# Kernel tuning notes

Hardware: AMD Instinct MI355X
Metric: run time of the kernel (lower is better)

Reference implementation:

```python
import jax, jax.numpy as jnp
import numpy as np

H, W, C = 768, 768, 64


def _segment_ids(mask):
    """mask: [L] int binary separator mask -> [L] int32 segment ids.
    A new grid segment starts at each rising edge (0 -> 1) of the mask;
    pixel 0 always belongs to segment 0. Equivalent to GridStructureBuilder's
    run-based row/column partition, derived via a single cumsum."""
    m = mask.astype(jnp.int32)
    prev = jnp.concatenate([jnp.zeros((1,), jnp.int32), m[:-1]])
    rising = ((m == 1) & (prev == 0)).at[0].set(False)
    return jnp.cumsum(rising.astype(jnp.int32))


def setup_inputs() -> dict:
    key = jax.random.key(0)
    k1, k2, k3 = jax.random.split(key, 3)
    return {
        "input": jax.random.normal(k1, (1, H, W, C), dtype=jnp.float32),
        "h_mask": jax.random.randint(k2, (1, H), 0, 2, dtype=jnp.int32),
        "v_mask": jax.random.randint(k3, (1, W), 0, 2, dtype=jnp.int32),
    }


def reference(input, h_mask, v_mask):
    x = input[0]                      # [H, W, C]
    h, w, c = x.shape
    row_ids = _segment_ids(h_mask[0])  # [H]
    col_ids = _segment_ids(v_mask[0])  # [W]
    # flat cell id per pixel; w is a static upper bound on the column count
    idx = (row_ids[:, None] * w + col_ids[None, :]).reshape(-1)  # [H*W]
    xf = x.reshape(h * w, c)
    n_seg = h * w                      # static upper bound on cell count
    sums = jax.ops.segment_sum(xf, idx, num_segments=n_seg)           # [n_seg, C]
    counts = jax.ops.segment_sum(jnp.ones((h * w,), x.dtype), idx,
                                 num_segments=n_seg)                  # [n_seg]
    # scatter-add of (1/area)*x == per-cell mean
    means = sums / jnp.maximum(counts, 1.0)[:, None]
    # keep_size=True: gather cell means back to every pixel
    return means[idx].reshape(1, h, w, c)
```

## Files before the change

kernel.cpp:

```cpp
#include <hip/hip_runtime.h>


#define GH 768
#define GW 768
#define GC 64
#define MAXSEG 385

enum {
    OFF_ROWSTART = 0,
    OFF_ROWEND   = OFF_ROWSTART + MAXSEG,
    OFF_COLSTART = OFF_ROWEND + MAXSEG,
    OFF_COLEND   = OFF_COLSTART + MAXSEG,
    OFF_NROWS    = OFF_COLEND + MAXSEG,
    OFF_NCOLS    = OFF_NROWS + 1,
};

__global__ __launch_bounds__(768) void seg_scan(const int* __restrict__ h_mask,
                                                const int* __restrict__ v_mask,
                                                int* __restrict__ ws) {
    __shared__ int s[GH];
    const int i = threadIdx.x;
    const bool is_row = (blockIdx.x == 0);
    const int* m = is_row ? h_mask : v_mask;

    int mi = m[i];
    int rising = 0;
    if (i > 0) rising = (mi == 1 && m[i - 1] == 0) ? 1 : 0;
    s[i] = rising;
    __syncthreads();

    for (int off = 1; off < GH; off <<= 1) {
        int add = (i >= off) ? s[i - off] : 0;
        __syncthreads();
        s[i] += add;
        __syncthreads();
    }

    const int seg  = s[i];
    const int segL = (i == 0)      ? -1 : s[i - 1];
    const int segR = (i == GH - 1) ? -2 : s[i + 1];

    int* start = ws + (is_row ? OFF_ROWSTART : OFF_COLSTART);
    int* end   = ws + (is_row ? OFF_ROWEND   : OFF_COLEND);
    if (seg != segL) start[seg] = i;
    if (seg != segR) end[seg]   = i + 1;
    if (i == GH - 1) ws[is_row ? OFF_NROWS : OFF_NCOLS] = seg + 1;
}

__global__ __launch_bounds__(256) void cell_pool(const float* __restrict__ in,
                                                 float* __restrict__ out,
                                                 const int* __restrict__ ws) {
    const int nrows = ws[OFF_NROWS];
    const int ncols = ws[OFF_NCOLS];
    const int br = blockIdx.y;
    const int bc = blockIdx.x;
    if (br >= nrows || bc >= ncols) return;

    const int y0 = ws[OFF_ROWSTART + br];
    const int y1 = ws[OFF_ROWEND + br];
    const int x0 = ws[OFF_COLSTART + bc];
    const int x1 = ws[OFF_COLEND + bc];
    const int wdt = x1 - x0;

    const int tid = threadIdx.x;
    const int c = tid & 63;
    const int g = tid >> 6;

    float acc = 0.f;
    for (int y = y0; y < y1; ++y) {
        const float* rowp = in + ((size_t)(y * GW + x0)) * GC + c;
        for (int x = g; x < wdt; x += 4) acc += rowp[(size_t)x * GC];
    }

    __shared__ float sred[256];
    sred[tid] = acc;
    __syncthreads();
    if (g == 0) {
        float sum = sred[c] + sred[c + 64] + sred[c + 128] + sred[c + 192];
        float area = (float)((y1 - y0) * wdt);
        sred[c] = sum / area;
    }
    __syncthreads();
    const float mval = sred[c];

    for (int y = y0; y < y1; ++y) {
        float* rowp = out + ((size_t)(y * GW + x0)) * GC + c;
        for (int x = g; x < wdt; x += 4) rowp[(size_t)x * GC] = mval;
    }
}

extern "C" void kernel_launch(void* const* d_in, const int* in_sizes, int n_in,
                              void* d_out, int out_size, void* d_ws, size_t ws_size,
                              hipStream_t stream) {
    const float* in  = (const float*)d_in[0];
    const int* hmask = (const int*)d_in[1];
    const int* vmask = (const int*)d_in[2];
    float* out = (float*)d_out;
    int* ws = (int*)d_ws;

    seg_scan<<<2, GH, 0, stream>>>(hmask, vmask, ws);
    dim3 grid(MAXSEG, MAXSEG);
    cell_pool<<<grid, 256, 0, stream>>>(in, out, ws);
}
```

Baseline: 313.0 us.

## Use one wave per cell with float4 accesses and a grid-stride loop

Cell pooling now assigns one 64-lane wave per grid cell instead of one 256-thread block per cell. Each lane handles four channels through float4 loads and stores, and the per-cell reduction uses xor shuffles instead of shared memory and barriers. A persistent grid of 2048 blocks strides over the actual cell count, so the fixed 385x385 grid with many early-exiting blocks goes away. The trade-off is that large cells are now processed by a single wave, which can leave work unevenly balanced.

```diff
diff --git a/kernel.cpp b/kernel.cpp
--- a/kernel.cpp
+++ b/kernel.cpp
@@ -47,45 +47,53 @@
     if (i == GH - 1) ws[is_row ? OFF_NROWS : OFF_NCOLS] = seg + 1;
 }
 
-__global__ __launch_bounds__(256) void cell_pool(const float* __restrict__ in,
-                                                 float* __restrict__ out,
+__global__ __launch_bounds__(256) void cell_pool(const float4* __restrict__ in,
+                                                 float4* __restrict__ out,
                                                  const int* __restrict__ ws) {
-    const int nrows = ws[OFF_NROWS];
-    const int ncols = ws[OFF_NCOLS];
-    const int br = blockIdx.y;
-    const int bc = blockIdx.x;
-    if (br >= nrows || bc >= ncols) return;
+    const int nrows  = ws[OFF_NROWS];
+    const int ncols  = ws[OFF_NCOLS];
+    const int ncells = nrows * ncols;
 
-    const int y0 = ws[OFF_ROWSTART + br];
-    const int y1 = ws[OFF_ROWEND + br];
-    const int x0 = ws[OFF_COLSTART + bc];
-    const int x1 = ws[OFF_COLEND + bc];
-    const int wdt = x1 - x0;
+    const int wave   = blockIdx.x * 4 + (threadIdx.x >> 6);
+    const int nwaves = gridDim.x * 4;
+    const int lane   = threadIdx.x & 63;
+    const int pg     = lane >> 4;
+    const int cq     = lane & 15;
 
-    const int tid = threadIdx.x;
-    const int c = tid & 63;
-    const int g = tid >> 6;
+    for (int cell = wave; cell < ncells; cell += nwaves) {
+        const int br = cell / ncols;
+        const int bc = cell - br * ncols;
+        const int y0 = ws[OFF_ROWSTART + br];
+        const int y1 = ws[OFF_ROWEND + br];
+        const int x0 = ws[OFF_COLSTART + bc];
+        const int x1 = ws[OFF_COLEND + bc];
 
-    float acc = 0.f;
-    for (int y = y0; y < y1; ++y) {
-        const float* rowp = in + ((size_t)(y * GW + x0)) * GC + c;
-        for (int x = g; x < wdt; x += 4) acc += rowp[(size_t)x * GC];
-    }
+        float4 acc = make_float4(0.f, 0.f, 0.f, 0.f);
+        for (int y = y0; y < y1; ++y) {
+            const size_t rb = (size_t)(y * GW) * 16 + cq;
+            for (int x = x0 + pg; x < x1; x += 4) {
+                float4 v = in[rb + (size_t)x * 16];
+                acc.x += v.x; acc.y += v.y; acc.z += v.z; acc.w += v.w;
+            }
+        }
+        #pragma unroll
+        for (int msk = 16; msk < 64; msk <<= 1) {
+            acc.x += __shfl_xor(acc.x, msk, 64);
+            acc.y += __shfl_xor(acc.y, msk, 64);
+            acc.z += __shfl_xor(acc.z, msk, 64);
+            acc.w += __shfl_xor(acc.w, msk, 64);
+        }
+        const float area = (float)((y1 - y0) * (x1 - x0));
+        float4 mean;
+        mean.x = acc.x / area; mean.y = acc.y / area;
+        mean.z = acc.z / area; mean.w = acc.w / area;
 
-    __shared__ float sred[256];
-    sred[tid] = acc;
-    __syncthreads();
-    if (g == 0) {
-        float sum = sred[c] + sred[c + 64] + sred[c + 128] + sred[c + 192];
-        float area = (float)((y1 - y0) * wdt);
-        sred[c] = sum / area;
-    }
-    __syncthreads();
-    const float mval = sred[c];
-
-    for (int y = y0; y < y1; ++y) {
-        float* rowp = out + ((size_t)(y * GW + x0)) * GC + c;
-        for (int x = g; x < wdt; x += 4) rowp[(size_t)x * GC] = mval;
+        for (int y = y0; y < y1; ++y) {
+            const size_t rb = (size_t)(y * GW) * 16 + cq;
+            for (int x = x0 + pg; x < x1; x += 4) {
+                out[rb + (size_t)x * 16] = mean;
+            }
+        }
     }
 }
 
@@ -99,6 +107,5 @@
     int* ws = (int*)d_ws;
 
     seg_scan<<<2, GH, 0, stream>>>(hmask, vmask, ws);
-    dim3 grid(MAXSEG, MAXSEG);
-    cell_pool<<<grid, 256, 0, stream>>>(in, out, ws);
+    cell_pool<<<2048, 256, 0, stream>>>((const float4*)in, (float4*)out, ws);
 }
```

New measurement: 282.0 us. 9.9% less time.
